# Kernel optimization log

Measured on AMD Instinct MI355X. Metric: run time of the kernel, lower is better.

## Reference

```python
import jax, jax.numpy as jnp
import numpy as np
from jax import lax

D_MODEL = 1024
D_STATE = 16
BATCH = 4
SEQ = 2048
EPS = 1e-5


def setup_inputs() -> dict:
    key = jax.random.key(0)
    ks = jax.random.split(key, 5)
    x = jax.random.normal(ks[0], (BATCH, SEQ, D_MODEL), dtype=jnp.float32)
    A_log = jax.random.normal(ks[1], (D_MODEL, D_STATE), dtype=jnp.float32) * 0.1
    # nn.Linear default init ~ U(-1/sqrt(fan_in), 1/sqrt(fan_in))
    B_w = jax.random.uniform(ks[2], (D_STATE, D_MODEL), minval=-1.0, maxval=1.0) / np.sqrt(D_MODEL)
    C_w = jax.random.uniform(ks[3], (D_MODEL, D_STATE), minval=-1.0, maxval=1.0) / np.sqrt(D_STATE)
    D = jnp.ones((D_MODEL,), dtype=jnp.float32)
    gamma = jnp.ones((D_MODEL,), dtype=jnp.float32)
    beta = jnp.zeros((D_MODEL,), dtype=jnp.float32)
    return {"x": x, "A_log": A_log, "B_w": B_w, "C_w": C_w, "D": D, "gamma": gamma, "beta": beta}


def _layernorm(y, gamma, beta):
    mu = jnp.mean(y, axis=-1, keepdims=True)
    var = jnp.mean((y - mu) ** 2, axis=-1, keepdims=True)
    return (y - mu) * lax.rsqrt(var + EPS) * gamma + beta


def reference(x, A_log, B_w, C_w, D, gamma, beta):
    batch, seq_len, d = x.shape
    decay = jnp.exp(-jnp.exp(A_log))  # (d_model, d_state), exp(A) with A = -exp(A_log)
    # Precompute all B projections: (batch, seq, d_state)
    bx = jnp.einsum('bsd,nd->bsn', x, B_w)
    bx_t = jnp.swapaxes(bx, 0, 1)  # (seq, batch, d_state)

    def step(h, b_t):
        # h: (batch, d_model, d_state); b_t broadcast over d_model dim
        h = h * decay + b_t[:, None, :]
        return h, h.mean(axis=1)  # carry, per-step mean (batch, d_state)

    h0 = jnp.zeros((batch, d, A_log.shape[1]), dtype=x.dtype)
    _, hmeans = lax.scan(step, h0, bx_t)  # hmeans: (seq, batch, d_state)

    y = jnp.einsum('sbn,dn->bsd', hmeans, C_w) + D * x  # (batch, seq, d_model)
    return _layernorm(y, gamma, beta)
```

## Files before the change

kernel.cpp:

```cpp
#include <hip/hip_runtime.h>
#include <hip/hip_bf16.h>

#define D_MODEL 1024
#define D_STATE 16
#define BATCH   4
#define SEQ     2048
#define ROWS    (BATCH*SEQ)
#define WIN     64

#define K1_ROWS 8
__global__ __launch_bounds__(256, 4) void k_proj(const float* __restrict__ x,
                                                 const float* __restrict__ Bw,
                                                 const float* __restrict__ A_log,
                                                 float* __restrict__ bx,
                                                 float* __restrict__ KbarT) {
    __shared__ float xs[K1_ROWS][1024];
    __shared__ float red[4][8][K1_ROWS][2];
    const int tid = threadIdx.x;

    if (blockIdx.x >= ROWS / K1_ROWS) {
        const int n = blockIdx.x - ROWS / K1_ROWS;
        float* l2   = &xs[0][0];
        float* kred = &xs[1][0];
        const int delta = tid & 63;
        const int c     = tid >> 6;
        for (int d = tid; d < D_MODEL; d += 256) {
            float a = A_log[d * D_STATE + n];
            l2[d] = -expf(a) * 1.4426950408889634f;
        }
        __syncthreads();
        const float fdelta = (float)delta;
        float acc = 0.f;
        const int d0 = c * 256;
        for (int d = d0; d < d0 + 256; ++d)
            acc += exp2f(fdelta * l2[d]);
        kred[c * WIN + delta] = acc;
        __syncthreads();
        if (tid < WIN)
            KbarT[tid * D_STATE + n] =
                (kred[tid] + kred[WIN + tid] + kred[2 * WIN + tid] + kred[3 * WIN + tid])
                * (1.0f / 1024.0f);
        return;
    }

    const int np   = tid & 7;
    const int dblk = tid >> 3;
    const int row0 = blockIdx.x * K1_ROWS;
    const int lane = tid & 63, wid = tid >> 6;

    float4 bw0[8], bw1[8];
    {
        const float4* p0 = reinterpret_cast<const float4*>(Bw + (size_t)(2 * np    ) * 1024 + dblk * 32);
        const float4* p1 = reinterpret_cast<const float4*>(Bw + (size_t)(2 * np + 1) * 1024 + dblk * 32);
#pragma unroll
        for (int j = 0; j < 8; ++j) { bw0[j] = p0[j]; bw1[j] = p1[j]; }
    }

    const int chunk = tid >> 3;
    const int slotw = ((tid & 7) + chunk) & 7;
#pragma unroll
    for (int r = 0; r < K1_ROWS; ++r) {
        float4 v = reinterpret_cast<const float4*>(x + (size_t)(row0 + r) * 1024)[tid];
        *reinterpret_cast<float4*>(&xs[r][chunk * 32 + slotw * 4]) = v;
    }
    __syncthreads();

    float a0[K1_ROWS], a1[K1_ROWS];
#pragma unroll
    for (int r = 0; r < K1_ROWS; ++r) { a0[r] = 0.f; a1[r] = 0.f; }

#pragma unroll
    for (int r = 0; r < K1_ROWS; ++r) {
#pragma unroll
        for (int j = 0; j < 8; ++j) {
            const int slot = (j + dblk) & 7;
            float4 xv = *reinterpret_cast<const float4*>(&xs[r][dblk * 32 + slot * 4]);
            a0[r] = fmaf(xv.x, bw0[j].x, a0[r]); a0[r] = fmaf(xv.y, bw0[j].y, a0[r]);
            a0[r] = fmaf(xv.z, bw0[j].z, a0[r]); a0[r] = fmaf(xv.w, bw0[j].w, a0[r]);
            a1[r] = fmaf(xv.x, bw1[j].x, a1[r]); a1[r] = fmaf(xv.y, bw1[j].y, a1[r]);
            a1[r] = fmaf(xv.z, bw1[j].z, a1[r]); a1[r] = fmaf(xv.w, bw1[j].w, a1[r]);
        }
    }

#pragma unroll
    for (int r = 0; r < K1_ROWS; ++r) {
        float v0 = a0[r], v1 = a1[r];
        v0 += __shfl_xor(v0, 8);  v1 += __shfl_xor(v1, 8);
        v0 += __shfl_xor(v0, 16); v1 += __shfl_xor(v1, 16);
        v0 += __shfl_xor(v0, 32); v1 += __shfl_xor(v1, 32);
        a0[r] = v0; a1[r] = v1;
    }
    if (lane < 8) {
#pragma unroll
        for (int r = 0; r < K1_ROWS; ++r) {
            red[wid][lane][r][0] = a0[r];
            red[wid][lane][r][1] = a1[r];
        }
    }
    __syncthreads();
    if (tid < K1_ROWS * 16) {
        const int r = tid >> 4, n = tid & 15;
        float v = red[0][n >> 1][r][n & 1] + red[1][n >> 1][r][n & 1]
                + red[2][n >> 1][r][n & 1] + red[3][n >> 1][r][n & 1];
        bx[(size_t)(row0 + r) * D_STATE + n] = v;
    }
}

__global__ __launch_bounds__(256) void k_fir(const float* __restrict__ bx,
                                             const float* __restrict__ KbarT,
                                             float* __restrict__ hm) {
    __shared__ float4 kb4[WIN][4];
    const int tid = threadIdx.x;
    kb4[tid >> 2][tid & 3] = reinterpret_cast<const float4*>(KbarT)[tid];
    __syncthreads();

    const int nq  = tid & 3;
    const int row = blockIdx.x * 64 + (tid >> 2);
    const int t   = row & (SEQ - 1);
    const float4* bp = reinterpret_cast<const float4*>(bx + (size_t)row * D_STATE) + nq;
    float4 acc = {0.f, 0.f, 0.f, 0.f};
    if (t >= WIN - 1) {
#pragma unroll
        for (int dl = 0; dl < WIN; ++dl) {
            float4 b = bp[-(ptrdiff_t)dl * 4];
            float4 k = kb4[dl][nq];
            acc.x = fmaf(k.x, b.x, acc.x); acc.y = fmaf(k.y, b.y, acc.y);
            acc.z = fmaf(k.z, b.z, acc.z); acc.w = fmaf(k.w, b.w, acc.w);
        }
    } else {
        for (int dl = 0; dl <= t; ++dl) {
            float4 b = bp[-(ptrdiff_t)dl * 4];
            float4 k = kb4[dl][nq];
            acc.x = fmaf(k.x, b.x, acc.x); acc.y = fmaf(k.y, b.y, acc.y);
            acc.z = fmaf(k.z, b.z, acc.z); acc.w = fmaf(k.w, b.w, acc.w);
        }
    }
    reinterpret_cast<float4*>(hm + (size_t)row * D_STATE)[nq] = acc;
}

#define KO_ROWS 8
__global__ __launch_bounds__(256, 4) void k_out(const float* __restrict__ x,
                                                const float* __restrict__ hm,
                                                const float* __restrict__ Cw,
                                                const float* __restrict__ Dp,
                                                const float* __restrict__ gamma,
                                                const float* __restrict__ beta,
                                                float* __restrict__ out) {
    const int tid = threadIdx.x;
    const int row0 = blockIdx.x * KO_ROWS;
    const int lane = tid & 63, wid = tid >> 6;
    __shared__ float red_s[2][4][4], red_q[2][4][4];

    float4 cw[4][4];
#pragma unroll
    for (int j = 0; j < 4; ++j) {
        const float4* p = reinterpret_cast<const float4*>(Cw + (size_t)(tid * 4 + j) * D_STATE);
#pragma unroll
        for (int q = 0; q < 4; ++q) cw[j][q] = p[q];
    }
    const float4 Dq = reinterpret_cast<const float4*>(Dp)[tid];
    const float4 gq = reinterpret_cast<const float4*>(gamma)[tid];
    const float4 bq = reinterpret_cast<const float4*>(beta)[tid];

    for (int h = 0; h < 2; ++h) {
        float4 y[4];
#pragma unroll
        for (int rr = 0; rr < 4; ++rr) {
            const size_t row = row0 + h * 4 + rr;
            const float4* hp = reinterpret_cast<const float4*>(hm + row * D_STATE);
            const float4 h0 = hp[0], h1 = hp[1], h2 = hp[2], h3 = hp[3];
            const float4 xq = reinterpret_cast<const float4*>(x + row * D_MODEL)[tid];

            float4 v;
#pragma unroll
            for (int j = 0; j < 4; ++j) {
                float a = 0.f;
                a = fmaf(h0.x, cw[j][0].x, a); a = fmaf(h0.y, cw[j][0].y, a);
                a = fmaf(h0.z, cw[j][0].z, a); a = fmaf(h0.w, cw[j][0].w, a);
                a = fmaf(h1.x, cw[j][1].x, a); a = fmaf(h1.y, cw[j][1].y, a);
                a = fmaf(h1.z, cw[j][1].z, a); a = fmaf(h1.w, cw[j][1].w, a);
                a = fmaf(h2.x, cw[j][2].x, a); a = fmaf(h2.y, cw[j][2].y, a);
                a = fmaf(h2.z, cw[j][2].z, a); a = fmaf(h2.w, cw[j][2].w, a);
                a = fmaf(h3.x, cw[j][3].x, a); a = fmaf(h3.y, cw[j][3].y, a);
                a = fmaf(h3.z, cw[j][3].z, a); a = fmaf(h3.w, cw[j][3].w, a);
                ((float*)&v)[j] = a;
            }
            v.x = fmaf(Dq.x, xq.x, v.x);
            v.y = fmaf(Dq.y, xq.y, v.y);
            v.z = fmaf(Dq.z, xq.z, v.z);
            v.w = fmaf(Dq.w, xq.w, v.w);
            y[rr] = v;

            float s  = v.x + v.y + v.z + v.w;
            float sq = v.x*v.x + v.y*v.y + v.z*v.z + v.w*v.w;
            s += __shfl_xor(s, 1);  sq += __shfl_xor(sq, 1);
            s += __shfl_xor(s, 2);  sq += __shfl_xor(sq, 2);
            s += __shfl_xor(s, 4);  sq += __shfl_xor(sq, 4);
            s += __shfl_xor(s, 8);  sq += __shfl_xor(sq, 8);
            s += __shfl_xor(s, 16); sq += __shfl_xor(sq, 16);
            s += __shfl_xor(s, 32); sq += __shfl_xor(sq, 32);
            if (lane == 0) { red_s[h][rr][wid] = s; red_q[h][rr][wid] = sq; }
        }
        __syncthreads();

#pragma unroll
        for (int rr = 0; rr < 4; ++rr) {
            const size_t row = row0 + h * 4 + rr;
            const float ssum = red_s[h][rr][0] + red_s[h][rr][1] + red_s[h][rr][2] + red_s[h][rr][3];
            const float ssq  = red_q[h][rr][0] + red_q[h][rr][1] + red_q[h][rr][2] + red_q[h][rr][3];
            const float mu   = ssum * (1.0f / 1024.0f);
            const float var  = ssq * (1.0f / 1024.0f) - mu * mu;
            const float inv  = rsqrtf(var + 1e-5f);
            const float4 v = y[rr];
            float4 o;
            o.x = fmaf((v.x - mu) * inv, gq.x, bq.x);
            o.y = fmaf((v.y - mu) * inv, gq.y, bq.y);
            o.z = fmaf((v.z - mu) * inv, gq.z, bq.z);
            o.w = fmaf((v.w - mu) * inv, gq.w, bq.w);
            reinterpret_cast<float4*>(out + row * D_MODEL)[tid] = o;
        }
    }
}

extern "C" void kernel_launch(void* const* d_in, const int* in_sizes, int n_in,
                              void* d_out, int out_size, void* d_ws, size_t ws_size,
                              hipStream_t stream) {
    (void)in_sizes; (void)n_in; (void)out_size; (void)ws_size;
    const float* x     = (const float*)d_in[0];
    const float* A_log = (const float*)d_in[1];
    const float* B_w   = (const float*)d_in[2];
    const float* C_w   = (const float*)d_in[3];
    const float* Dp    = (const float*)d_in[4];
    const float* gamma = (const float*)d_in[5];
    const float* beta  = (const float*)d_in[6];
    float* out = (float*)d_out;

    float* bx = (float*)d_ws;
    float* kb = bx + (size_t)ROWS * D_STATE;
    float* hm = kb + WIN * D_STATE;

    k_proj<<<ROWS / K1_ROWS + D_STATE, 256, 0, stream>>>(x, B_w, A_log, bx, kb);
    k_fir <<<ROWS / 64,               256, 0, stream>>>(bx, kb, hm);
    k_out <<<ROWS / KO_ROWS,          256, 0, stream>>>(x, hm, C_w, Dp, gamma, beta, out);
}
```

Baseline: 59.53 us.

## Fuse truncated FIR convolution into output/LayerNorm kernel

Removes the separate FIR kernel and computes the windowed convolution of the B-projections inside the output kernel. Each block stages a 71-row window of bx and the decay kernel in shared memory, splits the 64 taps across 8 thread groups and combines them with shuffles. This drops one launch and the hm round trip through global memory. In exchange, each block redundantly loads overlapping bx windows and adds an extra synchronisation before the LayerNorm work.

```diff
diff --git a/kernel.cpp b/kernel.cpp
--- a/kernel.cpp
+++ b/kernel.cpp
@@ -106,50 +106,69 @@
     }
 }
 
-__global__ __launch_bounds__(256) void k_fir(const float* __restrict__ bx,
-                                             const float* __restrict__ KbarT,
-                                             float* __restrict__ hm) {
-    __shared__ float4 kb4[WIN][4];
-    const int tid = threadIdx.x;
-    kb4[tid >> 2][tid & 3] = reinterpret_cast<const float4*>(KbarT)[tid];
-    __syncthreads();
-
-    const int nq  = tid & 3;
-    const int row = blockIdx.x * 64 + (tid >> 2);
-    const int t   = row & (SEQ - 1);
-    const float4* bp = reinterpret_cast<const float4*>(bx + (size_t)row * D_STATE) + nq;
-    float4 acc = {0.f, 0.f, 0.f, 0.f};
-    if (t >= WIN - 1) {
-#pragma unroll
-        for (int dl = 0; dl < WIN; ++dl) {
-            float4 b = bp[-(ptrdiff_t)dl * 4];
-            float4 k = kb4[dl][nq];
-            acc.x = fmaf(k.x, b.x, acc.x); acc.y = fmaf(k.y, b.y, acc.y);
-            acc.z = fmaf(k.z, b.z, acc.z); acc.w = fmaf(k.w, b.w, acc.w);
-        }
-    } else {
-        for (int dl = 0; dl <= t; ++dl) {
-            float4 b = bp[-(ptrdiff_t)dl * 4];
-            float4 k = kb4[dl][nq];
-            acc.x = fmaf(k.x, b.x, acc.x); acc.y = fmaf(k.y, b.y, acc.y);
-            acc.z = fmaf(k.z, b.z, acc.z); acc.w = fmaf(k.w, b.w, acc.w);
-        }
-    }
-    reinterpret_cast<float4*>(hm + (size_t)row * D_STATE)[nq] = acc;
-}
-
 #define KO_ROWS 8
-__global__ __launch_bounds__(256, 4) void k_out(const float* __restrict__ x,
-                                                const float* __restrict__ hm,
-                                                const float* __restrict__ Cw,
-                                                const float* __restrict__ Dp,
-                                                const float* __restrict__ gamma,
-                                                const float* __restrict__ beta,
-                                                float* __restrict__ out) {
+__global__ __launch_bounds__(256, 4) void k_tail(const float* __restrict__ x,
+                                                 const float* __restrict__ bxg,
+                                                 const float* __restrict__ KbarT,
+                                                 const float* __restrict__ Cw,
+                                                 const float* __restrict__ Dp,
+                                                 const float* __restrict__ gamma,
+                                                 const float* __restrict__ beta,
+                                                 float* __restrict__ out) {
     const int tid = threadIdx.x;
     const int row0 = blockIdx.x * KO_ROWS;
     const int lane = tid & 63, wid = tid >> 6;
+    __shared__ float4 bwin[71][4];
+    __shared__ float4 kb4[WIN][4];
+    __shared__ float4 hm4[KO_ROWS][4];
     __shared__ float red_s[2][4][4], red_q[2][4][4];
+
+    kb4[tid >> 2][tid & 3] = reinterpret_cast<const float4*>(KbarT)[tid];
+    const float4* bx4 = reinterpret_cast<const float4*>(bxg);
+    for (int f = tid; f < 71 * 4; f += 256) {
+        const int j = f >> 2, q = f & 3;
+        long g = (long)row0 - 63 + j;
+        if (g < 0) g = 0;
+        bwin[j][q] = bx4[g * 4 + q];
+    }
+    __syncthreads();
+
+    {
+        const int r_f = tid >> 5, dc = (tid >> 2) & 7, nq = tid & 3;
+        const int t0 = row0 & (SEQ - 1);
+        float4 acc = {0.f, 0.f, 0.f, 0.f};
+        if (t0 >= WIN) {
+#pragma unroll
+            for (int j = 0; j < 8; ++j) {
+                const int delta = dc * 8 + j;
+                const float4 b = bwin[63 + r_f - delta][nq];
+                const float4 k = kb4[delta][nq];
+                acc.x = fmaf(k.x, b.x, acc.x); acc.y = fmaf(k.y, b.y, acc.y);
+                acc.z = fmaf(k.z, b.z, acc.z); acc.w = fmaf(k.w, b.w, acc.w);
+            }
+        } else {
+            const int t = t0 + r_f;
+#pragma unroll
+            for (int j = 0; j < 8; ++j) {
+                const int delta = dc * 8 + j;
+                if (delta <= t) {
+                    const float4 b = bwin[63 + r_f - delta][nq];
+                    const float4 k = kb4[delta][nq];
+                    acc.x = fmaf(k.x, b.x, acc.x); acc.y = fmaf(k.y, b.y, acc.y);
+                    acc.z = fmaf(k.z, b.z, acc.z); acc.w = fmaf(k.w, b.w, acc.w);
+                }
+            }
+        }
+#pragma unroll
+        for (int off = 4; off <= 16; off <<= 1) {
+            acc.x += __shfl_xor(acc.x, off);
+            acc.y += __shfl_xor(acc.y, off);
+            acc.z += __shfl_xor(acc.z, off);
+            acc.w += __shfl_xor(acc.w, off);
+        }
+        if (dc == 0) hm4[r_f][nq] = acc;
+    }
+    __syncthreads();
 
     float4 cw[4][4];
 #pragma unroll
@@ -166,9 +185,9 @@
         float4 y[4];
 #pragma unroll
         for (int rr = 0; rr < 4; ++rr) {
-            const size_t row = row0 + h * 4 + rr;
-            const float4* hp = reinterpret_cast<const float4*>(hm + row * D_STATE);
-            const float4 h0 = hp[0], h1 = hp[1], h2 = hp[2], h3 = hp[3];
+            const int r = h * 4 + rr;
+            const size_t row = row0 + r;
+            const float4 h0 = hm4[r][0], h1 = hm4[r][1], h2 = hm4[r][2], h3 = hm4[r][3];
             const float4 xq = reinterpret_cast<const float4*>(x + row * D_MODEL)[tid];
 
             float4 v;
@@ -205,7 +224,8 @@
 
 #pragma unroll
         for (int rr = 0; rr < 4; ++rr) {
-            const size_t row = row0 + h * 4 + rr;
+            const int r = h * 4 + rr;
+            const size_t row = row0 + r;
             const float ssum = red_s[h][rr][0] + red_s[h][rr][1] + red_s[h][rr][2] + red_s[h][rr][3];
             const float ssq  = red_q[h][rr][0] + red_q[h][rr][1] + red_q[h][rr][2] + red_q[h][rr][3];
             const float mu   = ssum * (1.0f / 1024.0f);
@@ -237,9 +257,7 @@
 
     float* bx = (float*)d_ws;
     float* kb = bx + (size_t)ROWS * D_STATE;
-    float* hm = kb + WIN * D_STATE;
 
     k_proj<<<ROWS / K1_ROWS + D_STATE, 256, 0, stream>>>(x, B_w, A_log, bx, kb);
-    k_fir <<<ROWS / 64,               256, 0, stream>>>(bx, kb, hm);
-    k_out <<<ROWS / KO_ROWS,          256, 0, stream>>>(x, hm, C_w, Dp, gamma, beta, out);
+    k_tail<<<ROWS / KO_ROWS,           256, 0, stream>>>(x, bx, kb, C_w, Dp, gamma, beta, out);
 }
```

New measurement: 56.83 us. 1.05x faster.
